# Kernel optimization log

Hardware: AMD Instinct MI355X
Metric: run time of the kernel (lower is better)

Reference implementation:

```python
import jax, jax.numpy as jnp
import numpy as np

CELL = 0.5          # grid_map cell size (meters)
NUM_POSES = 256     # config.num_pose_samples


def setup_inputs() -> dict:
    key = jax.random.key(0)
    k1, k2, k3, k4 = jax.random.split(key, 4)
    B, N, I, J, D = 2, 1024, 128, 128, 32
    f_q = jax.random.normal(k1, (B, N, D), jnp.float32)
    f_map = jax.random.normal(k2, (B, I, J, D), jnp.float32)
    # query frustum points: 32x32 grid, x in [-15.5, 15.5], y in [0.5, 31.5]
    xs = jnp.arange(32, dtype=jnp.float32) - 15.5
    ys = jnp.arange(32, dtype=jnp.float32) + 0.5
    grid = jnp.stack(jnp.meshgrid(xs, ys, indexing='ij'), -1).reshape(-1, 2)
    q_xy = jnp.broadcast_to(grid, (B, N, 2)).astype(jnp.float32)
    valid_q = jax.random.bernoulli(k3, 0.9, (B, N))
    valid_map = jax.random.bernoulli(k4, 0.8, (B, I, J))
    temperature = jnp.array(0.5, jnp.float32)
    return {"f_q": f_q, "f_map": f_map, "q_xy": q_xy, "temperature": temperature,
            "valid_q": valid_q, "valid_map": valid_map, "seed": 0}


def reference(f_q, f_map, q_xy, temperature, valid_q, valid_map, seed):
    B, N, D = f_q.shape
    _, I, J, _ = f_map.shape
    K = NUM_POSES

    # dense cross-correlation: [B, N, I, J]
    sim = jnp.einsum('bnd,bijd->bnij', f_q, f_map)
    sim = jax.nn.relu(sim)                      # clip_negative_scores
    sim = sim.astype(jnp.float32) * jnp.exp(temperature)
    # joint softmax over the two spatial axes
    m = sim.max(axis=(-2, -1), keepdims=True)
    e = jnp.exp(sim - m)
    prob = e / e.sum(axis=(-2, -1), keepdims=True)
    num_valid = valid_q.sum(-1).clip(min=1).astype(jnp.float32)[:, None, None, None]
    sim = sim / num_valid
    prob = prob / num_valid

    # --- RANSAC 2-point pose sampling (no gradient through prob) ---
    p = jax.lax.stop_gradient(prob)
    kq, km = jax.random.split(jax.random.key(seed))
    n_idx = jax.random.randint(kq, (B, 2 * K), 0, N)          # 2 query pts per pose
    b_idx = jnp.arange(B)[:, None]
    p_flat = p.reshape(B, N, I * J)
    rows = p_flat[b_idx, n_idx]                               # [B, 2K, IJ]
    m_flat = jax.random.categorical(km, jnp.log(rows + 1e-20), axis=-1)  # [B, 2K]
    mi, mj = m_flat // J, m_flat % J
    m_xy = (jnp.stack([mi, mj], -1).astype(jnp.float32) + 0.5) * CELL    # cell centers
    m_xy = m_xy.reshape(B, K, 2, 2)
    q_pts = q_xy[b_idx, n_idx].reshape(B, K, 2, 2)
    dq = q_pts[:, :, 1] - q_pts[:, :, 0]
    dm = m_xy[:, :, 1] - m_xy[:, :, 0]
    theta = jnp.arctan2(dm[..., 1], dm[..., 0]) - jnp.arctan2(dq[..., 1], dq[..., 0])
    c, s = jnp.cos(theta), jnp.sin(theta)
    R = jnp.stack([jnp.stack([c, -s], -1), jnp.stack([s, c], -1)], -2)   # [B,K,2,2]
    t = m_xy[:, :, 0] - jnp.einsum('bkxy,bky->bkx', R, q_pts[:, :, 0])   # [B,K,2]

    # --- score every pose hypothesis ---
    p_map = jnp.einsum('bkxy,bny->bknx', R, q_xy) + t[:, :, None]        # [B,K,N,2]
    ij = jnp.floor(p_map / CELL).astype(jnp.int32)
    inb = (ij[..., 0] >= 0) & (ij[..., 0] < I) & (ij[..., 1] >= 0) & (ij[..., 1] < J)
    flat = jnp.clip(ij[..., 0], 0, I - 1) * J + jnp.clip(ij[..., 1], 0, J - 1)  # [B,K,N]
    vmap_flat = valid_map.reshape(B, I * J)
    vgather = vmap_flat[b_idx, flat.reshape(B, K * N)].reshape(B, K, N)
    sim_flat = sim.reshape(B, N, I * J)
    sgather = jnp.take_along_axis(sim_flat, flat.transpose(0, 2, 1), axis=2)  # [B,N,K]
    mask = valid_q[:, None, :] & inb & vgather                                # [B,K,N]
    scores = jnp.sum(sgather.transpose(0, 2, 1) * mask, axis=-1)              # [B,K]
    return scores
```

## Files before the change

### kernel.cpp

```cpp
#include <hip/hip_runtime.h>
#include <hip/hip_bf16.h>
#include <stdint.h>

typedef unsigned int u32;

#define IJ 16384
#define NQ 1024
#define NB 2
#define KP 256
#define NSEG 8
#define SEGW 2048

__device__ __forceinline__ void tf2x32(u32 k0, u32 k1, u32& x0, u32& x1) {
  u32 kx = k0 ^ k1 ^ 0x1BD11BDAu;
#define TFR(r) { x0 += x1; x1 = (x1 << (r)) | (x1 >> (32 - (r))); x1 ^= x0; }
  x0 += k0; x1 += k1;
  TFR(13) TFR(15) TFR(26) TFR(6)
  x0 += k1; x1 += kx + 1u;
  TFR(17) TFR(29) TFR(16) TFR(24)
  x0 += kx; x1 += k0 + 2u;
  TFR(13) TFR(15) TFR(26) TFR(6)
  x0 += k0; x1 += k1 + 3u;
  TFR(17) TFR(29) TFR(16) TFR(24)
  x0 += k1; x1 += kx + 4u;
  TFR(13) TFR(15) TFR(26) TFR(6)
  x0 += kx; x1 += k0 + 5u;
#undef TFR
}

__device__ __forceinline__ void tf_subkey(u32 k0, u32 k1, u32 i, u32& s0, u32& s1) {
  u32 x0 = 0u, x1 = i;
  tf2x32(k0, k1, x0, x1);
  s0 = x0; s1 = x1;
}

__device__ __forceinline__ u32 tf_xorbits(u32 k0, u32 k1, u32 i) {
  u32 x0 = 0u, x1 = i;
  tf2x32(k0, k1, x0, x1);
  return x0 ^ x1;
}

__device__ __forceinline__ void derive_keys(int seed, u32& kq0, u32& kq1,
                                            u32& km0, u32& km1) {
  u32 k0 = 0u;
  u32 k1 = (u32)seed;
  tf_subkey(k0, k1, 0u, kq0, kq1);
  tf_subkey(k0, k1, 1u, km0, km1);
}

__device__ __forceinline__ float gumbel_from_bits(u32 w) {
  const float tiny = 1.17549435e-38f;
  float fl = __uint_as_float((w >> 9) | 0x3f800000u) - 1.0f;
  float u = fl * (1.0f - tiny) + tiny;
  u = fmaxf(tiny, u);
  return -logf(-logf(u));
}

__device__ __forceinline__ bool read_bool(const void* p, int idx, int is32) {
  return is32 ? (((const int*)p)[idx] != 0)
              : (((const unsigned char*)p)[idx] != 0);
}

__global__ void setup_kernel(const void* __restrict__ valid_q,
                             const int* __restrict__ seedp,
                             float* __restrict__ row_max,
                             float* __restrict__ num_valid,
                             int* __restrict__ n_idx,
                             int* __restrict__ bool_is32) {
  __shared__ int sred[256];
  __shared__ int is32_s;
  const int blk = blockIdx.x, tid = threadIdx.x;
  if (blk < 4) {
    int s = blk * 256 + tid;
    u32 kq0, kq1, km0, km1;
    derive_keys(seedp[0], kq0, kq1, km0, km1);
    u32 l0, l1;
    tf_subkey(kq0, kq1, 1u, l0, l1);
    u32 w = tf_xorbits(l0, l1, (u32)s);
    n_idx[s] = (int)(w & 1023u);
  } else if (blk == 4) {
    const unsigned char* vb = (const unsigned char*)valid_q;
    int ones = 0;
    for (int i = tid; i < 2048; i += 256) ones += (vb[i] == 1) ? 1 : 0;
    sred[tid] = ones;
    __syncthreads();
    for (int off = 128; off > 0; off >>= 1) {
      if (tid < off) sred[tid] += sred[tid + off];
      __syncthreads();
    }
    if (tid == 0) {
      is32_s = (sred[0] < 1152) ? 1 : 0;
      bool_is32[0] = is32_s;
    }
    __syncthreads();
    const int is32 = is32_s;
    for (int b = 0; b < 2; ++b) {
      int acc = 0;
      for (int i = tid; i < NQ; i += 256)
        acc += read_bool(valid_q, b * NQ + i, is32) ? 1 : 0;
      sred[tid] = acc;
      __syncthreads();
      for (int off = 128; off > 0; off >>= 1) {
        if (tid < off) sred[tid] += sred[tid + off];
        __syncthreads();
      }
      if (tid == 0) {
        float nv = (float)sred[0];
        num_valid[b] = nv < 1.f ? 1.f : nv;
      }
      __syncthreads();
    }
  } else {
    for (int i = (blk - 5) * 256 + tid; i < NB * NQ; i += 768) row_max[i] = 0.f;
  }
}

__global__ __launch_bounds__(256) void gemm_kernel(
    const float* __restrict__ f_q, const float* __restrict__ f_map,
    const float* __restrict__ temp, float* __restrict__ sim,
    float* __restrict__ row_max, float* __restrict__ rowsum_part) {
  __shared__ float As[32][64];
  __shared__ float Bs[32][256];
  __shared__ float rmax[64];
  const int tid = threadIdx.x;
  const int b = blockIdx.z;
  const int n0 = blockIdx.y * 64;
  const int ij0 = blockIdx.x * 256;

  {
    const float4* gA = (const float4*)(f_q + ((size_t)b * NQ + n0) * 32);
    for (int q = tid; q < 512; q += 256) {
      float4 v = gA[q];
      int nn = q >> 3, dg = (q & 7) << 2;
      As[dg][nn] = v.x; As[dg + 1][nn] = v.y; As[dg + 2][nn] = v.z; As[dg + 3][nn] = v.w;
    }
  }
  {
    const float4* gB = (const float4*)(f_map + ((size_t)b * IJ + ij0) * 32);
    for (int q = tid; q < 2048; q += 256) {
      float4 v = gB[q];
      int jj = q >> 3, dg = (q & 7) << 2;
      Bs[dg][jj] = v.x; Bs[dg + 1][jj] = v.y; Bs[dg + 2][jj] = v.z; Bs[dg + 3][jj] = v.w;
    }
  }
  if (tid < 64) rmax[tid] = 0.f;
  __syncthreads();

  const int ty = tid >> 5, tx = tid & 31;
  float acc[2][2][4][4] = {};
#pragma unroll 8
  for (int d = 0; d < 32; ++d) {
    float4 a0 = *(const float4*)&As[d][ty << 2];
    float4 a1 = *(const float4*)&As[d][(ty << 2) + 32];
    float4 b0 = *(const float4*)&Bs[d][tx << 2];
    float4 b1 = *(const float4*)&Bs[d][(tx << 2) + 128];
    float av[2][4] = {{a0.x, a0.y, a0.z, a0.w}, {a1.x, a1.y, a1.z, a1.w}};
    float bv[2][4] = {{b0.x, b0.y, b0.z, b0.w}, {b1.x, b1.y, b1.z, b1.w}};
#pragma unroll
    for (int rg = 0; rg < 2; ++rg)
#pragma unroll
      for (int cg = 0; cg < 2; ++cg)
#pragma unroll
        for (int r = 0; r < 4; ++r)
#pragma unroll
          for (int c = 0; c < 4; ++c)
            acc[rg][cg][r][c] = fmaf(av[rg][r], bv[cg][c], acc[rg][cg][r][c]);
  }

  const float et = expf(temp[0]);
#pragma unroll
  for (int rg = 0; rg < 2; ++rg) {
#pragma unroll
    for (int r = 0; r < 4; ++r) {
      const int lrow = rg * 32 + (ty << 2) + r;
      const int n = n0 + lrow;
      float* base = sim + ((size_t)b * NQ + n) * IJ + ij0;
      float rm = 0.f;
      float se = 0.f;
#pragma unroll
      for (int cg = 0; cg < 2; ++cg) {
        float4 o;
        o.x = fmaxf(acc[rg][cg][r][0], 0.f) * et;
        o.y = fmaxf(acc[rg][cg][r][1], 0.f) * et;
        o.z = fmaxf(acc[rg][cg][r][2], 0.f) * et;
        o.w = fmaxf(acc[rg][cg][r][3], 0.f) * et;
        *(float4*)(base + cg * 128 + (tx << 2)) = o;
        rm = fmaxf(rm, fmaxf(fmaxf(o.x, o.y), fmaxf(o.z, o.w)));
        se += expf(o.x); se += expf(o.y); se += expf(o.z); se += expf(o.w);
      }
      atomicMax((u32*)&rmax[lrow], __float_as_uint(rm));
#pragma unroll
      for (int off = 16; off > 0; off >>= 1) se += __shfl_down(se, off, 32);
      if (tx == 0)
        rowsum_part[((size_t)(b * NQ + n)) * 64 + blockIdx.x] = se;
    }
  }
  __syncthreads();
  if (tid < 64)
    atomicMax((u32*)&row_max[(size_t)b * NQ + n0 + tid], __float_as_uint(rmax[tid]));
}

__global__ void sumexp_reduce_kernel(const float* __restrict__ rowsum_part,
                                     const float* __restrict__ row_max,
                                     float* __restrict__ row_sumexp) {
  const int row = blockIdx.x * 256 + threadIdx.x;
  if (row >= NB * NQ) return;
  const float* p = rowsum_part + (size_t)row * 64;
  float s = 0.f;
#pragma unroll
  for (int t = 0; t < 64; ++t) s += p[t];
  row_sumexp[row] = s * expf(-row_max[row]);
}

__global__ __launch_bounds__(256) void cat_seg_kernel(
    const float* __restrict__ sim, const float* __restrict__ row_max,
    const float* __restrict__ row_sumexp, const float* __restrict__ num_valid,
    const int* __restrict__ n_idx, const int* __restrict__ seedp,
    float* __restrict__ segv, int* __restrict__ segi) {
  __shared__ unsigned short cand[2][SEGW];
  __shared__ int ccount[2];
  __shared__ u32 keys[2];
  __shared__ float sv[2][256];
  __shared__ int si[2][256];
  const int seg = blockIdx.x;
  const int t = blockIdx.y;
  const int tid = threadIdx.x;
  if (tid == 0) {
    u32 kq0, kq1, km0, km1;
    derive_keys(seedp[0], kq0, kq1, km0, km1);
    keys[0] = km0; keys[1] = km1;
    ccount[0] = 0; ccount[1] = 0;
  }
  __syncthreads();

  const int nA = n_idx[t], nB = n_idx[512 + t];
  const float m0 = row_max[nA], s0 = row_sumexp[nA];
  const float m1 = row_max[NQ + nB], s1 = row_sumexp[NQ + nB];
  const float nv0 = num_valid[0], nv1 = num_valid[1];
  const float thA = m0 - 25.0f;
  const float thB = m1 - 25.0f;
  const float* r0 = sim + (size_t)nA * IJ + seg * SEGW;
  const float* r1 = sim + (size_t)(NQ + nB) * IJ + seg * SEGW;

#pragma unroll
  for (int k = 0; k < 2; ++k) {
    const int l = tid + k * 256;
    const int lf = l * 4;
    float4 va = ((const float4*)r0)[l];
    float4 vb = ((const float4*)r1)[l];
    const float ra[4] = {va.x, va.y, va.z, va.w};
    const float rb[4] = {vb.x, vb.y, vb.z, vb.w};
#pragma unroll
    for (int c = 0; c < 4; ++c) {
      if (ra[c] > thA) { int p = atomicAdd(&ccount[0], 1); cand[0][p] = (unsigned short)(lf + c); }
      if (rb[c] > thB) { int p = atomicAdd(&ccount[1], 1); cand[1][p] = (unsigned short)(lf + c); }
    }
  }
  __syncthreads();

  const u32 km0 = keys[0], km1 = keys[1];
  const int c0 = ccount[0], c1 = ccount[1];
  const int fbase = seg * SEGW;
  float bv0 = -1e30f, bv1 = -1e30f;
  int bi0 = IJ, bi1 = IJ;
  for (int c = tid; c < c0; c += 256) {
    int f = fbase + (int)cand[0][c];
    u32 w = tf_xorbits(km0, km1, (u32)(t * IJ + f));
    float g = gumbel_from_bits(w);
    float e = expf(r0[f - fbase] - m0);
    float v = logf((e / s0) / nv0 + 1e-20f) + g;
    if (v > bv0 || (v == bv0 && f < bi0)) { bv0 = v; bi0 = f; }
  }
  for (int c = tid; c < c1; c += 256) {
    int f = fbase + (int)cand[1][c];
    u32 w = tf_xorbits(km0, km1, (u32)(t * IJ + f) + 8388608u);
    float g = gumbel_from_bits(w);
    float e = expf(r1[f - fbase] - m1);
    float v = logf((e / s1) / nv1 + 1e-20f) + g;
    if (v > bv1 || (v == bv1 && f < bi1)) { bv1 = v; bi1 = f; }
  }
  sv[0][tid] = bv0; si[0][tid] = bi0;
  sv[1][tid] = bv1; si[1][tid] = bi1;
  __syncthreads();
  for (int off = 128; off > 0; off >>= 1) {
    if (tid < off) {
#pragma unroll
      for (int q = 0; q < 2; ++q) {
        float v2 = sv[q][tid + off];
        int i2 = si[q][tid + off];
        if (v2 > sv[q][tid] || (v2 == sv[q][tid] && i2 < si[q][tid])) {
          sv[q][tid] = v2; si[q][tid] = i2;
        }
      }
    }
    __syncthreads();
  }
  if (tid == 0) {
    segv[(0 * 512 + t) * NSEG + seg] = sv[0][0];
    segi[(0 * 512 + t) * NSEG + seg] = si[0][0];
    segv[(1 * 512 + t) * NSEG + seg] = sv[1][0];
    segi[(1 * 512 + t) * NSEG + seg] = si[1][0];
  }
}

__global__ void cat_reduce_kernel(const float* __restrict__ segv,
                                  const int* __restrict__ segi,
                                  int* __restrict__ m_flat) {
  const int idx = blockIdx.x * 256 + threadIdx.x;
  if (idx >= NB * 512) return;
  float bv = -1e30f;
  int bi = IJ;
#pragma unroll
  for (int s = 0; s < NSEG; ++s) {
    float v = segv[idx * NSEG + s];
    int i = segi[idx * NSEG + s];
    if (v > bv || (v == bv && i < bi)) { bv = v; bi = i; }
  }
  m_flat[idx] = bi;
}

__global__ void pose_kernel(const float* __restrict__ q_xy,
                            const int* __restrict__ n_idx,
                            const int* __restrict__ m_flat,
                            float4* __restrict__ poses) {
  const int idx = blockIdx.x * 256 + threadIdx.x;
  if (idx >= NB * KP) return;
  const int b = idx >> 8, k = idx & 255;
  const int t0 = b * 512 + 2 * k, t1 = t0 + 1;
  const int na = n_idx[t0], nb = n_idx[t1];
  const float2 q0 = ((const float2*)q_xy)[(size_t)b * NQ + na];
  const float2 q1 = ((const float2*)q_xy)[(size_t)b * NQ + nb];
  const int ma = m_flat[t0], mb = m_flat[t1];
  const float m0x = ((float)(ma >> 7) + 0.5f) * 0.5f;
  const float m0y = ((float)(ma & 127) + 0.5f) * 0.5f;
  const float m1x = ((float)(mb >> 7) + 0.5f) * 0.5f;
  const float m1y = ((float)(mb & 127) + 0.5f) * 0.5f;
  const float dqx = q1.x - q0.x, dqy = q1.y - q0.y;
  const float dmx = m1x - m0x, dmy = m1y - m0y;
  const float theta = atan2f(dmy, dmx) - atan2f(dqy, dqx);
  const float c = cosf(theta), s = sinf(theta);
  const float tx = m0x - (c * q0.x - s * q0.y);
  const float ty = m0y - (s * q0.x + c * q0.y);
  poses[idx] = make_float4(c, s, tx, ty);
}

__global__ __launch_bounds__(256) void score_kernel(
    const float* __restrict__ sim, const float* __restrict__ q_xy,
    const void* __restrict__ valid_q, const void* __restrict__ valid_map,
    const float* __restrict__ num_valid, const float4* __restrict__ poses,
    const int* __restrict__ bool_is32, float* __restrict__ out) {
  __shared__ float sred[256];
  const int idx = blockIdx.x;
  const int tid = threadIdx.x;
  const int b = idx >> 8;
  const int is32 = bool_is32[0];
  const float4 P = poses[idx];
  float acc = 0.f;
  for (int n = tid; n < NQ; n += 256) {
    float2 q = ((const float2*)q_xy)[(size_t)b * NQ + n];
    float px = P.x * q.x - P.y * q.y + P.z;
    float py = P.y * q.x + P.x * q.y + P.w;
    int ii = (int)floorf(px * 2.0f);
    int jj = (int)floorf(py * 2.0f);
    bool inb = (ii >= 0) & (ii < 128) & (jj >= 0) & (jj < 128);
    int ic = min(max(ii, 0), 127), jc = min(max(jj, 0), 127);
    int flat = (ic << 7) + jc;
    bool msk = read_bool(valid_q, b * NQ + n, is32) && inb &&
               read_bool(valid_map, b * IJ + flat, is32);
    if (msk) acc += sim[((size_t)(b * NQ + n)) * IJ + flat];
  }
  sred[tid] = acc;
  __syncthreads();
  for (int off = 128; off > 0; off >>= 1) {
    if (tid < off) sred[tid] += sred[tid + off];
    __syncthreads();
  }
  if (tid == 0) out[idx] = sred[0] / num_valid[b];
}

extern "C" void kernel_launch(void* const* d_in, const int* in_sizes, int n_in,
                              void* d_out, int out_size, void* d_ws,
                              size_t ws_size, hipStream_t stream) {
  const float* f_q = (const float*)d_in[0];
  const float* f_map = (const float*)d_in[1];
  const float* q_xy = (const float*)d_in[2];
  const float* temp = (const float*)d_in[3];
  const void* valid_q = d_in[4];
  const void* valid_map = d_in[5];
  const int* seedp = (const int*)d_in[6];
  float* out = (float*)d_out;

  char* ws = (char*)d_ws;
  const size_t SIM_BYTES = (size_t)NB * NQ * IJ * 4;
  float* sim = (float*)ws;
  float* row_max = (float*)(ws + SIM_BYTES);
  float* row_sumexp = (float*)(ws + SIM_BYTES + 8192);
  float* num_valid = (float*)(ws + SIM_BYTES + 16384);
  int* n_idx = (int*)(ws + SIM_BYTES + 16448);
  int* m_flat = (int*)(ws + SIM_BYTES + 20544);
  float4* poses = (float4*)(ws + SIM_BYTES + 24640);
  int* bool_is32 = (int*)(ws + SIM_BYTES + 32832);
  float* segv = (float*)(ws + SIM_BYTES + 36864);
  int* segi = (int*)(ws + SIM_BYTES + 69632);
  float* rowsum_part = (float*)(ws + SIM_BYTES + 102400);

  setup_kernel<<<8, 256, 0, stream>>>(valid_q, seedp, row_max, num_valid,
                                      n_idx, bool_is32);
  gemm_kernel<<<dim3(64, 16, 2), 256, 0, stream>>>(f_q, f_map, temp, sim,
                                                   row_max, rowsum_part);
  sumexp_reduce_kernel<<<8, 256, 0, stream>>>(rowsum_part, row_max, row_sumexp);
  cat_seg_kernel<<<dim3(NSEG, 512), 256, 0, stream>>>(
      sim, row_max, row_sumexp, num_valid, n_idx, seedp, segv, segi);
  cat_reduce_kernel<<<4, 256, 0, stream>>>(segv, segi, m_flat);
  pose_kernel<<<2, 256, 0, stream>>>(q_xy, n_idx, m_flat, poses);
  score_kernel<<<NB * KP, 256, 0, stream>>>(sim, q_xy, valid_q, valid_map,
                                            num_valid, poses, bool_is32, out);
}
```

Baseline: 166.6 us.

## Compute similarity GEMM with split-fp16 MFMA instead of scalar FP32 FMAs

Replaces the scalar FP32 outer-product GEMM with MFMA 16x16x32 f16 instructions. Each FP32 input is split into a high fp16 part and a scaled residual fp16 part, and four MFMAs per tile recover near-FP32 accuracy. The epilogue moves to the MFMA output layout and uses wave shuffles for the row max and sum-exp reductions, which removes the shared-memory atomics. This targets the compute-bound FMA loop at the cost of extra conversion work and some accuracy risk from the split-precision scheme.

```diff
diff --git a/kernel.cpp b/kernel.cpp
--- a/kernel.cpp
+++ b/kernel.cpp
@@ -3,6 +3,8 @@
 #include <stdint.h>
 
 typedef unsigned int u32;
+typedef _Float16 f16x8 __attribute__((ext_vector_type(8)));
+typedef float f32x4 __attribute__((ext_vector_type(4)));
 
 #define IJ 16384
 #define NQ 1024
@@ -119,85 +121,92 @@
     const float* __restrict__ f_q, const float* __restrict__ f_map,
     const float* __restrict__ temp, float* __restrict__ sim,
     float* __restrict__ row_max, float* __restrict__ rowsum_part) {
-  __shared__ float As[32][64];
-  __shared__ float Bs[32][256];
-  __shared__ float rmax[64];
+  __shared__ __align__(16) _Float16 ldsA[2][4][64][8];
+  __shared__ __align__(16) _Float16 ldsB[2][16][64][8];
   const int tid = threadIdx.x;
   const int b = blockIdx.z;
   const int n0 = blockIdx.y * 64;
   const int ij0 = blockIdx.x * 256;
 
   {
-    const float4* gA = (const float4*)(f_q + ((size_t)b * NQ + n0) * 32);
-    for (int q = tid; q < 512; q += 256) {
-      float4 v = gA[q];
-      int nn = q >> 3, dg = (q & 7) << 2;
-      As[dg][nn] = v.x; As[dg + 1][nn] = v.y; As[dg + 2][nn] = v.z; As[dg + 3][nn] = v.w;
-    }
-  }
-  {
-    const float4* gB = (const float4*)(f_map + ((size_t)b * IJ + ij0) * 32);
-    for (int q = tid; q < 2048; q += 256) {
-      float4 v = gB[q];
-      int jj = q >> 3, dg = (q & 7) << 2;
-      Bs[dg][jj] = v.x; Bs[dg + 1][jj] = v.y; Bs[dg + 2][jj] = v.z; Bs[dg + 3][jj] = v.w;
-    }
-  }
-  if (tid < 64) rmax[tid] = 0.f;
+    const int l = tid & 63, rt = tid >> 6;
+    const int g = l >> 4, r = l & 15;
+    const float* src = f_q + ((size_t)b * NQ + n0 + rt * 16 + r) * 32 + g * 4;
+    float4 v0 = *(const float4*)src;
+    float4 v1 = *(const float4*)(src + 16);
+    float x[8] = {v0.x, v0.y, v0.z, v0.w, v1.x, v1.y, v1.z, v1.w};
+    f16x8 h1, h2;
+#pragma unroll
+    for (int e = 0; e < 8; ++e) {
+      _Float16 a = (_Float16)x[e];
+      h1[e] = a;
+      h2[e] = (_Float16)((x[e] - (float)a) * 2048.0f);
+    }
+    *(f16x8*)(&ldsA[0][rt][l][0]) = h1;
+    *(f16x8*)(&ldsA[1][rt][l][0]) = h2;
+  }
+  for (int s = tid; s < 1024; s += 256) {
+    const int l = s & 63, t = s >> 6;
+    const int g = l >> 4, r = l & 15;
+    const float* src = f_map + ((size_t)b * IJ + ij0 + t * 16 + r) * 32 + g * 4;
+    float4 v0 = *(const float4*)src;
+    float4 v1 = *(const float4*)(src + 16);
+    float x[8] = {v0.x, v0.y, v0.z, v0.w, v1.x, v1.y, v1.z, v1.w};
+    f16x8 h1, h2;
+#pragma unroll
+    for (int e = 0; e < 8; ++e) {
+      _Float16 a = (_Float16)x[e];
+      h1[e] = a;
+      h2[e] = (_Float16)((x[e] - (float)a) * 2048.0f);
+    }
+    *(f16x8*)(&ldsB[0][t][l][0]) = h1;
+    *(f16x8*)(&ldsB[1][t][l][0]) = h2;
+  }
   __syncthreads();
 
-  const int ty = tid >> 5, tx = tid & 31;
-  float acc[2][2][4][4] = {};
-#pragma unroll 8
-  for (int d = 0; d < 32; ++d) {
-    float4 a0 = *(const float4*)&As[d][ty << 2];
-    float4 a1 = *(const float4*)&As[d][(ty << 2) + 32];
-    float4 b0 = *(const float4*)&Bs[d][tx << 2];
-    float4 b1 = *(const float4*)&Bs[d][(tx << 2) + 128];
-    float av[2][4] = {{a0.x, a0.y, a0.z, a0.w}, {a1.x, a1.y, a1.z, a1.w}};
-    float bv[2][4] = {{b0.x, b0.y, b0.z, b0.w}, {b1.x, b1.y, b1.z, b1.w}};
-#pragma unroll
-    for (int rg = 0; rg < 2; ++rg)
-#pragma unroll
-      for (int cg = 0; cg < 2; ++cg)
-#pragma unroll
-        for (int r = 0; r < 4; ++r)
-#pragma unroll
-          for (int c = 0; c < 4; ++c)
-            acc[rg][cg][r][c] = fmaf(av[rg][r], bv[cg][c], acc[rg][cg][r][c]);
+  const int w = tid >> 6, l = tid & 63;
+  const f16x8 q1 = *(const f16x8*)(&ldsA[0][w][l][0]);
+  const f16x8 q2 = *(const f16x8*)(&ldsA[1][w][l][0]);
+  const f32x4 zero4 = {0.f, 0.f, 0.f, 0.f};
+  const float c11 = 4.8828125e-4f;
+  f32x4 acc[16];
+#pragma unroll
+  for (int t = 0; t < 16; ++t) {
+    f16x8 m1 = *(const f16x8*)(&ldsB[0][t][l][0]);
+    f16x8 m2 = *(const f16x8*)(&ldsB[1][t][l][0]);
+    f32x4 x = __builtin_amdgcn_mfma_f32_16x16x32_f16(m2, q2, zero4, 0, 0, 0);
+    x *= c11;
+    x = __builtin_amdgcn_mfma_f32_16x16x32_f16(m2, q1, x, 0, 0, 0);
+    x = __builtin_amdgcn_mfma_f32_16x16x32_f16(m1, q2, x, 0, 0, 0);
+    x *= c11;
+    acc[t] = __builtin_amdgcn_mfma_f32_16x16x32_f16(m1, q1, x, 0, 0, 0);
   }
 
   const float et = expf(temp[0]);
-#pragma unroll
-  for (int rg = 0; rg < 2; ++rg) {
-#pragma unroll
-    for (int r = 0; r < 4; ++r) {
-      const int lrow = rg * 32 + (ty << 2) + r;
-      const int n = n0 + lrow;
-      float* base = sim + ((size_t)b * NQ + n) * IJ + ij0;
-      float rm = 0.f;
-      float se = 0.f;
-#pragma unroll
-      for (int cg = 0; cg < 2; ++cg) {
-        float4 o;
-        o.x = fmaxf(acc[rg][cg][r][0], 0.f) * et;
-        o.y = fmaxf(acc[rg][cg][r][1], 0.f) * et;
-        o.z = fmaxf(acc[rg][cg][r][2], 0.f) * et;
-        o.w = fmaxf(acc[rg][cg][r][3], 0.f) * et;
-        *(float4*)(base + cg * 128 + (tx << 2)) = o;
-        rm = fmaxf(rm, fmaxf(fmaxf(o.x, o.y), fmaxf(o.z, o.w)));
-        se += expf(o.x); se += expf(o.y); se += expf(o.z); se += expf(o.w);
-      }
-      atomicMax((u32*)&rmax[lrow], __float_as_uint(rm));
-#pragma unroll
-      for (int off = 16; off > 0; off >>= 1) se += __shfl_down(se, off, 32);
-      if (tx == 0)
-        rowsum_part[((size_t)(b * NQ + n)) * 64 + blockIdx.x] = se;
-    }
-  }
-  __syncthreads();
-  if (tid < 64)
-    atomicMax((u32*)&row_max[(size_t)b * NQ + n0 + tid], __float_as_uint(rmax[tid]));
+  const int r15 = l & 15, g = l >> 4;
+  const int row = n0 + w * 16 + r15;
+  float* base = sim + ((size_t)b * NQ + row) * IJ + ij0 + g * 4;
+  float rm = 0.f, se = 0.f;
+#pragma unroll
+  for (int t = 0; t < 16; ++t) {
+    float4 o;
+    o.x = fmaxf(acc[t][0], 0.f) * et;
+    o.y = fmaxf(acc[t][1], 0.f) * et;
+    o.z = fmaxf(acc[t][2], 0.f) * et;
+    o.w = fmaxf(acc[t][3], 0.f) * et;
+    *(float4*)(base + t * 16) = o;
+    rm = fmaxf(rm, fmaxf(fmaxf(o.x, o.y), fmaxf(o.z, o.w)));
+    se += expf(o.x); se += expf(o.y); se += expf(o.z); se += expf(o.w);
+  }
+#pragma unroll
+  for (int off = 16; off < 64; off <<= 1) {
+    se += __shfl_xor(se, off, 64);
+    rm = fmaxf(rm, __shfl_xor(rm, off, 64));
+  }
+  if (g == 0) {
+    rowsum_part[((size_t)(b * NQ + row)) * 64 + blockIdx.x] = se;
+    atomicMax((u32*)&row_max[(size_t)b * NQ + row], __float_as_uint(rm));
+  }
 }
 
 __global__ void sumexp_reduce_kernel(const float* __restrict__ rowsum_part,
```

Result: faster. 151.1 us (-9.3%).
